# Kernel optimization log

Hardware: AMD Instinct MI355X
Metric: run time of the kernel (lower is better)

## Reference

```python
import jax, jax.numpy as jnp
import numpy as np

N_NODES = 100000


def gcn_conv(x, edge_index, W, b):
    """PyG GCNConv: symmetric normalization with added self-loops.
    x: [N, Fin], edge_index: [2, E], W: [Fin, Fout], b: [Fout]
    """
    n = x.shape[0]
    h = x @ W  # [N, Fout] dense transform first (standard GCNConv order)
    loops = jnp.arange(n, dtype=edge_index.dtype)
    src = jnp.concatenate([edge_index[0], loops])  # self-loops appended
    dst = jnp.concatenate([edge_index[1], loops])
    deg = jax.ops.segment_sum(jnp.ones_like(dst, dtype=h.dtype), dst, num_segments=n)
    dinv = jax.lax.rsqrt(deg)  # deg >= 1 thanks to self-loops
    norm = dinv[src] * dinv[dst]  # [E+N]
    msgs = h[src] * norm[:, None]  # gather + scale
    out = jax.ops.segment_sum(msgs, dst, num_segments=n)  # scatter-add
    return out + b


def setup_inputs() -> dict:
    key = jax.random.key(0)
    k = jax.random.split(key, 9)
    in_c, hid, out_c = 128, 128, 64
    n_edges = 1600000
    x = jax.random.normal(k[0], (N_NODES, in_c), dtype=jnp.float32)
    edge_index = jax.random.randint(k[1], (2, n_edges), 0, N_NODES, dtype=jnp.int64)
    def lin(kw, kb, fan_in, fan_out):
        bound = 1.0 / np.sqrt(fan_in)
        W = jax.random.uniform(kw, (fan_in, fan_out), jnp.float32, -bound, bound)
        b = jax.random.uniform(kb, (fan_out,), jnp.float32, -bound, bound)
        return W, b
    W1, b1 = lin(k[2], k[3], in_c, hid)
    W2, b2 = lin(k[4], k[5], hid, hid)
    Wf, bf = lin(k[6], k[7], hid, out_c)
    return {"x": x, "edge_index": edge_index, "W1": W1, "b1": b1,
            "W2": W2, "b2": b2, "Wf": Wf, "bf": bf}


def reference(x, edge_index, W1, b1, W2, b2, Wf, bf):
    h = jax.nn.relu(gcn_conv(x, edge_index, W1, b1))
    h = jax.nn.relu(gcn_conv(h, edge_index, W2, b2))
    return h @ Wf + bf
```

## Files before the change

kernel.cpp:

```cpp
#include <hip/hip_runtime.h>
#include <stdint.h>

typedef short short8 __attribute__((ext_vector_type(8)));
typedef float floatx4 __attribute__((ext_vector_type(4)));

#define BK 256

static __device__ __forceinline__ float bflo(unsigned int u) {
    union { unsigned int i; float f; } v; v.i = u << 16; return v.f;
}
static __device__ __forceinline__ float bfhi(unsigned int u) {
    union { unsigned int i; float f; } v; v.i = u & 0xffff0000u; return v.f;
}
static __device__ __forceinline__ unsigned short f2bf(float f) {
    union { float f; unsigned int i; } v; v.f = f;
    unsigned int u = v.i;
    unsigned int r = u + 0x7fffu + ((u >> 16) & 1u);
    return (unsigned short)(r >> 16);
}


__global__ void k_zero_cnt(int* bucket_cnt, int K) {
    int i = blockIdx.x * 256 + threadIdx.x;
    if (i < K) bucket_cnt[i] = 0;
}

__global__ __launch_bounds__(256) void k_hist(const int* __restrict__ dst, int* bucket_cnt,
                                              int E, int N, int K) {
    __shared__ int h[512];
    int t = threadIdx.x;
    for (int i = t; i < K; i += 256) h[i] = 0;
    __syncthreads();
    int per = (E + gridDim.x - 1) / gridDim.x;
    int lo = blockIdx.x * per, hi = min(lo + per, E);
    for (int e = lo + t; e < hi; e += 256) {
        unsigned int d = (unsigned int)dst[e];
        if (d < (unsigned int)N) atomicAdd(&h[d >> 8], 1);
    }
    __syncthreads();
    for (int i = t; i < K; i += 256) if (h[i]) atomicAdd(&bucket_cnt[i], h[i]);
}

__global__ void k_scanK(const int* __restrict__ bucket_cnt, int* bucket_off, int* bucket_cur,
                        int* row_start, int K, int N) {
    __shared__ int s[512];
    int t = threadIdx.x;
    int v = (t < K) ? bucket_cnt[t] : 0;
    s[t] = v; __syncthreads();
    for (int off = 1; off < 512; off <<= 1) {
        int x = (t >= off) ? s[t - off] : 0;
        __syncthreads();
        s[t] += x;
        __syncthreads();
    }
    if (t < K) { bucket_off[t] = s[t] - v; bucket_cur[t] = s[t] - v; }
    if (t == K - 1) { bucket_off[K] = s[t]; row_start[N] = s[t]; }
}

__global__ __launch_bounds__(256) void k_binscatter(const int* __restrict__ src,
                                                    const int* __restrict__ dst,
                                                    int* bucket_cur, uint2* __restrict__ tmp,
                                                    int E, int N, int K) {
    __shared__ int h[512];
    __shared__ int base[512];
    int t = threadIdx.x;
    for (int i = t; i < K; i += 256) h[i] = 0;
    __syncthreads();
    int per = (E + gridDim.x - 1) / gridDim.x;
    int lo = blockIdx.x * per, hi = min(lo + per, E);
    for (int e = lo + t; e < hi; e += 256) {
        unsigned int d = (unsigned int)dst[e], sv = (unsigned int)src[e];
        if (d < (unsigned int)N && sv < (unsigned int)N) atomicAdd(&h[d >> 8], 1);
    }
    __syncthreads();
    for (int i = t; i < K; i += 256) {
        int c = h[i];
        base[i] = c ? atomicAdd(&bucket_cur[i], c) : 0;
        h[i] = 0;
    }
    __syncthreads();
    for (int e = lo + t; e < hi; e += 256) {
        unsigned int d = (unsigned int)dst[e], sv = (unsigned int)src[e];
        if (d < (unsigned int)N && sv < (unsigned int)N) {
            int k = d >> 8;
            int p = base[k] + atomicAdd(&h[k], 1);
            tmp[p] = make_uint2(sv, d);
        }
    }
}

__global__ __launch_bounds__(256) void k_fine(const uint2* __restrict__ tmp,
                                              const int* __restrict__ bucket_off,
                                              int* __restrict__ row_start, float* __restrict__ dinv,
                                              int* __restrict__ csr, int N) {
    __shared__ int deg[BK];
    __shared__ int scn[BK];
    __shared__ int cur[BK];
    int b = blockIdx.x;
    int t = threadIdx.x;
    int lo = bucket_off[b], hi = bucket_off[b + 1];
    deg[t] = 0;
    __syncthreads();
    for (int e = lo + t; e < hi; e += 256) {
        int d = tmp[e].y & (BK - 1);
        atomicAdd(&deg[d], 1);
    }
    __syncthreads();
    int v = deg[t];
    scn[t] = v; __syncthreads();
    for (int off = 1; off < 256; off <<= 1) {
        int x = (t >= off) ? scn[t - off] : 0;
        __syncthreads();
        scn[t] += x;
        __syncthreads();
    }
    int rs = lo + scn[t] - v;
    cur[t] = rs;
    int node = b * BK + t;
    if (node < N) { row_start[node] = rs; dinv[node] = rsqrtf((float)(v + 1)); }
    __syncthreads();
    for (int e = lo + t; e < hi; e += 256) {
        uint2 ed = tmp[e];
        int d = ed.y & (BK - 1);
        int p = atomicAdd(&cur[d], 1);
        csr[p] = (int)ed.x;
    }
}


__global__ void k_wconv(const float* __restrict__ W, unsigned short* __restrict__ Wt,
                        int K, int Nc) {
    int i = blockIdx.x * 256 + threadIdx.x;
    if (i < K * Nc) {
        int k = i / Nc, n = i % Nc;
        Wt[n * K + k] = f2bf(W[i]);
    }
}


template <int NOUT, bool SCALE, bool BIAS, bool XF32, bool OUTF32>
__global__ __launch_bounds__(256, 2) void k_gemm(
    const void* __restrict__ Xv, const unsigned short* __restrict__ Wbf,
    const float* __restrict__ bias, const float* __restrict__ dinv,
    void* __restrict__ outv, int M, int MB) {
    __shared__ __align__(16) unsigned short Wl[NOUT * 136];
    int t = threadIdx.x;
    for (int c = t; c < NOUT * 16; c += 256) {
        short8 v = *(const short8*)(Wbf + (size_t)c * 8);
        *(short8*)(&Wl[(c >> 4) * 136 + (c & 15) * 8]) = v;
    }
    __syncthreads();

    int wave = t >> 6, lane = t & 63;
    int quad = lane >> 4, l16 = lane & 15;
    constexpr int NT = NOUT / 16;

    for (int mb = blockIdx.x; mb < MB; mb += gridDim.x) {
        int m0 = mb * 64 + wave * 16;
        int mr = m0 + l16;
        int mrc = mr < M ? mr : M - 1;

        floatx4 acc[NT];
#pragma unroll
        for (int i = 0; i < NT; i++) acc[i] = (floatx4){0.f, 0.f, 0.f, 0.f};

#pragma unroll
        for (int kc = 0; kc < 4; kc++) {
            short8 a;
            if (XF32) {
                const float* X = (const float*)Xv;
                const float* p = X + (size_t)mrc * 128 + kc * 32 + quad * 8;
                float4 xa = *(const float4*)p;
                float4 xb = *(const float4*)(p + 4);
                a[0] = (short)f2bf(xa.x); a[1] = (short)f2bf(xa.y);
                a[2] = (short)f2bf(xa.z); a[3] = (short)f2bf(xa.w);
                a[4] = (short)f2bf(xb.x); a[5] = (short)f2bf(xb.y);
                a[6] = (short)f2bf(xb.z); a[7] = (short)f2bf(xb.w);
            } else {
                const unsigned short* X = (const unsigned short*)Xv;
                a = *(const short8*)(X + (size_t)mrc * 128 + kc * 32 + quad * 8);
            }
#pragma unroll
            for (int nt = 0; nt < NT; nt++) {
                short8 b = *(const short8*)(&Wl[(nt * 16 + l16) * 136 + kc * 32 + quad * 8]);
                acc[nt] = __builtin_amdgcn_mfma_f32_16x16x32_bf16(a, b, acc[nt], 0, 0, 0);
            }
        }

#pragma unroll
        for (int i = 0; i < 4; i++) {
            int r = m0 + quad * 4 + i;
            if (r >= M) continue;
            float sc = SCALE ? dinv[r] : 1.0f;
#pragma unroll
            for (int nt = 0; nt < NT; nt++) {
                int n = nt * 16 + l16;
                float v = acc[nt][i] * sc;
                if (BIAS) v += bias[n];
                if (OUTF32) {
                    ((float*)outv)[(size_t)r * NOUT + n] = v;
                } else {
                    ((unsigned short*)outv)[(size_t)r * NOUT + n] = f2bf(v);
                }
            }
        }
    }
}


__global__ __launch_bounds__(256, 8) void k_aggregate(
    const unsigned short* __restrict__ Hs, const int* __restrict__ csr,
    const int* __restrict__ row_start,
    const float* __restrict__ dinv, const float* __restrict__ bias,
    unsigned short* __restrict__ out, int N, int E) {
    int wave = threadIdx.x >> 6, lane = threadIdx.x & 63;
    int node = blockIdx.x * 4 + wave;
    if (node >= N) return;
    int ch = lane * 2;
    int Nm1 = N - 1;

    unsigned int u = *(const unsigned int*)(Hs + (size_t)node * 128 + ch);
    float a0 = bflo(u), a1 = bfhi(u);

    int e = row_start[node];
    int end = row_start[node + 1];
    if (e < 0) e = 0;
    if (end > E) end = E;

    for (; e + 8 <= end; e += 8) {
        int idx[8];
#pragma unroll
        for (int j = 0; j < 8; j++) idx[j] = __builtin_nontemporal_load(csr + e + j);
        unsigned int uu[8];
#pragma unroll
        for (int j = 0; j < 8; j++) {
            int s = min(max(idx[j], 0), Nm1);
            uu[j] = *(const unsigned int*)(Hs + (size_t)s * 128 + ch);
        }
#pragma unroll
        for (int j = 0; j < 8; j++) { a0 += bflo(uu[j]); a1 += bfhi(uu[j]); }
    }
    if (e + 4 <= end) {
        int idx[4];
#pragma unroll
        for (int j = 0; j < 4; j++) idx[j] = __builtin_nontemporal_load(csr + e + j);
        unsigned int uu[4];
#pragma unroll
        for (int j = 0; j < 4; j++) {
            int s = min(max(idx[j], 0), Nm1);
            uu[j] = *(const unsigned int*)(Hs + (size_t)s * 128 + ch);
        }
#pragma unroll
        for (int j = 0; j < 4; j++) { a0 += bflo(uu[j]); a1 += bfhi(uu[j]); }
        e += 4;
    }
    for (; e < end; e++) {
        int s = min(max(__builtin_nontemporal_load(csr + e), 0), Nm1);
        unsigned int u0 = *(const unsigned int*)(Hs + (size_t)s * 128 + ch);
        a0 += bflo(u0);
        a1 += bfhi(u0);
    }

    float di = dinv[node];
    float r0 = fmaxf(fmaf(di, a0, bias[ch]), 0.f);
    float r1 = fmaxf(fmaf(di, a1, bias[ch + 1]), 0.f);
    unsigned int pk = (unsigned int)f2bf(r0) | ((unsigned int)f2bf(r1) << 16);
    __builtin_nontemporal_store(pk, (unsigned int*)(out + (size_t)node * 128 + ch));
}


extern "C" void kernel_launch(void* const* d_in, const int* in_sizes, int n_in,
                              void* d_out, int out_size, void* d_ws, size_t ws_size,
                              hipStream_t stream) {
    const float* x  = (const float*)d_in[0];
    const int* ei   = (const int*)d_in[1];
    const float* W1 = (const float*)d_in[2];
    const float* b1 = (const float*)d_in[3];
    const float* W2 = (const float*)d_in[4];
    const float* b2 = (const float*)d_in[5];
    const float* Wf = (const float*)d_in[6];
    const float* bf = (const float*)d_in[7];

    int N = in_sizes[0] / 128;
    int E = in_sizes[1] / 2;
    const int* src = ei;
    const int* dst = ei + E;
    int K = (N + BK - 1) / BK;

    size_t need = 0;
    auto pad = [](size_t b) { return (b + 255) & ~(size_t)255; };
    size_t o_bcnt = need; need += pad(512 * 4);
    size_t o_boff = need; need += pad(513 * 4);
    size_t o_bcur = need; need += pad(512 * 4);
    size_t o_rs   = need; need += pad(((size_t)N + 1) * 4);
    size_t o_dinv = need; need += pad((size_t)N * 4);
    size_t o_wbf  = need; need += pad((16384 + 16384 + 8192) * 2);
    size_t o_csr  = need; need += pad((size_t)E * 4);
    size_t o_hs   = need; need += pad((size_t)N * 128 * 2);
    size_t o_a    = need; need += pad((size_t)N * 128 * 2);
    if (ws_size < need) return;
    if ((size_t)E * 8 > (size_t)N * 128 * 2) return;

    char* ws = (char*)d_ws;
    int* bucket_cnt = (int*)(ws + o_bcnt);
    int* bucket_off = (int*)(ws + o_boff);
    int* bucket_cur = (int*)(ws + o_bcur);
    int* row_start  = (int*)(ws + o_rs);
    float* dinv     = (float*)(ws + o_dinv);
    unsigned short* wb1 = (unsigned short*)(ws + o_wbf);
    unsigned short* wb2 = wb1 + 16384;
    unsigned short* wbf = wb2 + 16384;
    int* csr        = (int*)(ws + o_csr);
    unsigned short* Hs = (unsigned short*)(ws + o_hs);
    unsigned short* A  = (unsigned short*)(ws + o_a);
    uint2* tmp      = (uint2*)A;

    k_wconv<<<64, 256, 0, stream>>>(W1, wb1, 128, 128);
    k_wconv<<<64, 256, 0, stream>>>(W2, wb2, 128, 128);
    k_wconv<<<32, 256, 0, stream>>>(Wf, wbf, 128, 64);

    k_zero_cnt<<<(K + 255) / 256, 256, 0, stream>>>(bucket_cnt, K);
    k_hist<<<256, 256, 0, stream>>>(dst, bucket_cnt, E, N, K);
    k_scanK<<<1, 512, 0, stream>>>(bucket_cnt, bucket_off, bucket_cur, row_start, K, N);
    k_binscatter<<<256, 256, 0, stream>>>(src, dst, bucket_cur, tmp, E, N, K);
    k_fine<<<K, 256, 0, stream>>>(tmp, bucket_off, row_start, dinv, csr, N);

    int MB = (N + 63) / 64;
    int GG = (MB + 1) / 2;

    k_gemm<128, true, false, true, false><<<GG, 256, 0, stream>>>(x, wb1, nullptr, dinv, Hs, N, MB);
    k_aggregate<<<(N + 3) / 4, 256, 0, stream>>>(Hs, csr, row_start, dinv, b1, A, N, E);
    k_gemm<128, true, false, false, false><<<GG, 256, 0, stream>>>(A, wb2, nullptr, dinv, Hs, N, MB);
    k_aggregate<<<(N + 3) / 4, 256, 0, stream>>>(Hs, csr, row_start, dinv, b2, A, N, E);
    k_gemm<64, false, true, false, true><<<GG, 256, 0, stream>>>(A, wbf, bf, nullptr, d_out, N, MB);
}
```

Baseline: 376.1 us.

## Pack edge temp to 32-bit, per-wave histograms, vectorized aggregate, fused weight conversion

The aggregate kernel now has each wave handle four edges at once. Each 16-lane group loads 16-byte chunks of a row, and the partial sums are combined with cross-lane shuffles, replacing one 4-byte load per lane per edge. The binning temp buffer is packed into one 32-bit word per edge (source<<8 | local dst) instead of an 8-byte pair, which halves the traffic in binscatter and fine. Histograms use per-wave shared-memory copies to reduce atomic contention. The three weight-conversion launches are merged into one. The shuffle reduction adds ALU work, and the packed format assumes N < 2^24.

```diff
diff --git a/kernel.cpp b/kernel.cpp
--- a/kernel.cpp
+++ b/kernel.cpp
@@ -27,18 +27,21 @@
 
 __global__ __launch_bounds__(256) void k_hist(const int* __restrict__ dst, int* bucket_cnt,
                                               int E, int N, int K) {
-    __shared__ int h[512];
-    int t = threadIdx.x;
-    for (int i = t; i < K; i += 256) h[i] = 0;
+    __shared__ int h[4][512];
+    int t = threadIdx.x, w = t >> 6;
+    for (int i = t; i < 4 * 512; i += 256) ((int*)h)[i] = 0;
     __syncthreads();
     int per = (E + gridDim.x - 1) / gridDim.x;
     int lo = blockIdx.x * per, hi = min(lo + per, E);
     for (int e = lo + t; e < hi; e += 256) {
         unsigned int d = (unsigned int)dst[e];
-        if (d < (unsigned int)N) atomicAdd(&h[d >> 8], 1);
-    }
-    __syncthreads();
-    for (int i = t; i < K; i += 256) if (h[i]) atomicAdd(&bucket_cnt[i], h[i]);
+        if (d < (unsigned int)N) atomicAdd(&h[w][d >> 8], 1);
+    }
+    __syncthreads();
+    for (int i = t; i < K; i += 256) {
+        int c = h[0][i] + h[1][i] + h[2][i] + h[3][i];
+        if (c) atomicAdd(&bucket_cnt[i], c);
+    }
 }
 
 __global__ void k_scanK(const int* __restrict__ bucket_cnt, int* bucket_off, int* bucket_cur,
@@ -59,54 +62,52 @@
 
 __global__ __launch_bounds__(256) void k_binscatter(const int* __restrict__ src,
                                                     const int* __restrict__ dst,
-                                                    int* bucket_cur, uint2* __restrict__ tmp,
+                                                    int* bucket_cur, unsigned int* __restrict__ tmp,
                                                     int E, int N, int K) {
-    __shared__ int h[512];
-    __shared__ int base[512];
-    int t = threadIdx.x;
-    for (int i = t; i < K; i += 256) h[i] = 0;
+    __shared__ int h[4][512];
+    int t = threadIdx.x, w = t >> 6;
+    for (int i = t; i < 4 * 512; i += 256) ((int*)h)[i] = 0;
     __syncthreads();
     int per = (E + gridDim.x - 1) / gridDim.x;
     int lo = blockIdx.x * per, hi = min(lo + per, E);
     for (int e = lo + t; e < hi; e += 256) {
-        unsigned int d = (unsigned int)dst[e], sv = (unsigned int)src[e];
-        if (d < (unsigned int)N && sv < (unsigned int)N) atomicAdd(&h[d >> 8], 1);
-    }
-    __syncthreads();
-    for (int i = t; i < K; i += 256) {
-        int c = h[i];
-        base[i] = c ? atomicAdd(&bucket_cur[i], c) : 0;
-        h[i] = 0;
+        unsigned int d = (unsigned int)dst[e];
+        if (d < (unsigned int)N) atomicAdd(&h[w][d >> 8], 1);
+    }
+    __syncthreads();
+    for (int k = t; k < K; k += 256) {
+        int c0 = h[0][k], c1 = h[1][k], c2 = h[2][k], c3 = h[3][k];
+        int tot = c0 + c1 + c2 + c3;
+        int base = tot ? atomicAdd(&bucket_cur[k], tot) : 0;
+        h[0][k] = base; h[1][k] = base + c0; h[2][k] = base + c0 + c1;
+        h[3][k] = base + c0 + c1 + c2;
     }
     __syncthreads();
     for (int e = lo + t; e < hi; e += 256) {
-        unsigned int d = (unsigned int)dst[e], sv = (unsigned int)src[e];
-        if (d < (unsigned int)N && sv < (unsigned int)N) {
-            int k = d >> 8;
-            int p = base[k] + atomicAdd(&h[k], 1);
-            tmp[p] = make_uint2(sv, d);
+        unsigned int d = (unsigned int)dst[e];
+        if (d < (unsigned int)N) {
+            unsigned int sv = (unsigned int)src[e];
+            if (sv >= (unsigned int)N) sv = 0;
+            int p = atomicAdd(&h[w][d >> 8], 1);
+            tmp[p] = (sv << 8) | (d & 255u);
         }
     }
 }
 
-__global__ __launch_bounds__(256) void k_fine(const uint2* __restrict__ tmp,
+__global__ __launch_bounds__(256) void k_fine(const unsigned int* __restrict__ tmp,
                                               const int* __restrict__ bucket_off,
                                               int* __restrict__ row_start, float* __restrict__ dinv,
                                               int* __restrict__ csr, int N) {
-    __shared__ int deg[BK];
+    __shared__ int deg4[4][BK];
     __shared__ int scn[BK];
     __shared__ int cur[BK];
-    int b = blockIdx.x;
-    int t = threadIdx.x;
+    int b = blockIdx.x, t = threadIdx.x, w = t >> 6;
     int lo = bucket_off[b], hi = bucket_off[b + 1];
-    deg[t] = 0;
-    __syncthreads();
-    for (int e = lo + t; e < hi; e += 256) {
-        int d = tmp[e].y & (BK - 1);
-        atomicAdd(&deg[d], 1);
-    }
-    __syncthreads();
-    int v = deg[t];
+    for (int i = t; i < 4 * BK; i += 256) ((int*)deg4)[i] = 0;
+    __syncthreads();
+    for (int e = lo + t; e < hi; e += 256) atomicAdd(&deg4[w][tmp[e] & 255u], 1);
+    __syncthreads();
+    int v = deg4[0][t] + deg4[1][t] + deg4[2][t] + deg4[3][t];
     scn[t] = v; __syncthreads();
     for (int off = 1; off < 256; off <<= 1) {
         int x = (t >= off) ? scn[t - off] : 0;
@@ -120,20 +121,26 @@
     if (node < N) { row_start[node] = rs; dinv[node] = rsqrtf((float)(v + 1)); }
     __syncthreads();
     for (int e = lo + t; e < hi; e += 256) {
-        uint2 ed = tmp[e];
-        int d = ed.y & (BK - 1);
-        int p = atomicAdd(&cur[d], 1);
-        csr[p] = (int)ed.x;
-    }
-}
-
-
-__global__ void k_wconv(const float* __restrict__ W, unsigned short* __restrict__ Wt,
-                        int K, int Nc) {
+        unsigned int p = tmp[e];
+        int pos = atomicAdd(&cur[p & 255u], 1);
+        csr[pos] = (int)(p >> 8);
+    }
+}
+
+
+__global__ void k_wconv_all(const float* __restrict__ W1, const float* __restrict__ W2,
+                            const float* __restrict__ Wf, unsigned short* __restrict__ wb1,
+                            unsigned short* __restrict__ wb2, unsigned short* __restrict__ wbf) {
     int i = blockIdx.x * 256 + threadIdx.x;
-    if (i < K * Nc) {
-        int k = i / Nc, n = i % Nc;
-        Wt[n * K + k] = f2bf(W[i]);
+    if (i < 16384) {
+        int k = i >> 7, n = i & 127;
+        wb1[n * 128 + k] = f2bf(W1[i]);
+    } else if (i < 32768) {
+        int j = i - 16384, k = j >> 7, n = j & 127;
+        wb2[n * 128 + k] = f2bf(W2[j]);
+    } else if (i < 40960) {
+        int j = i - 32768, k = j >> 6, n = j & 63;
+        wbf[n * 128 + k] = f2bf(Wf[j]);
     }
 }
 
@@ -214,58 +221,79 @@
     const float* __restrict__ dinv, const float* __restrict__ bias,
     unsigned short* __restrict__ out, int N, int E) {
     int wave = threadIdx.x >> 6, lane = threadIdx.x & 63;
+    int grp = lane >> 4, c16 = lane & 15;
     int node = blockIdx.x * 4 + wave;
     if (node >= N) return;
-    int ch = lane * 2;
     int Nm1 = N - 1;
-
-    unsigned int u = *(const unsigned int*)(Hs + (size_t)node * 128 + ch);
-    float a0 = bflo(u), a1 = bfhi(u);
-
-    int e = row_start[node];
+    int cb = c16 * 8;
+
+    float a0 = 0.f, a1 = 0.f, a2 = 0.f, a3 = 0.f, a4 = 0.f, a5 = 0.f, a6 = 0.f, a7 = 0.f;
+
+    int start = row_start[node];
     int end = row_start[node + 1];
-    if (e < 0) e = 0;
+    if (start < 0) start = 0;
     if (end > E) end = E;
-
-    for (; e + 8 <= end; e += 8) {
-        int idx[8];
-#pragma unroll
-        for (int j = 0; j < 8; j++) idx[j] = __builtin_nontemporal_load(csr + e + j);
-        unsigned int uu[8];
-#pragma unroll
-        for (int j = 0; j < 8; j++) {
-            int s = min(max(idx[j], 0), Nm1);
-            uu[j] = *(const unsigned int*)(Hs + (size_t)s * 128 + ch);
-        }
-#pragma unroll
-        for (int j = 0; j < 8; j++) { a0 += bflo(uu[j]); a1 += bfhi(uu[j]); }
-    }
-    if (e + 4 <= end) {
-        int idx[4];
-#pragma unroll
-        for (int j = 0; j < 4; j++) idx[j] = __builtin_nontemporal_load(csr + e + j);
-        unsigned int uu[4];
-#pragma unroll
-        for (int j = 0; j < 4; j++) {
-            int s = min(max(idx[j], 0), Nm1);
-            uu[j] = *(const unsigned int*)(Hs + (size_t)s * 128 + ch);
-        }
-#pragma unroll
-        for (int j = 0; j < 4; j++) { a0 += bflo(uu[j]); a1 += bfhi(uu[j]); }
-        e += 4;
-    }
-    for (; e < end; e++) {
-        int s = min(max(__builtin_nontemporal_load(csr + e), 0), Nm1);
-        unsigned int u0 = *(const unsigned int*)(Hs + (size_t)s * 128 + ch);
-        a0 += bflo(u0);
-        a1 += bfhi(u0);
-    }
+    int cnt = end - start;
+    int full4 = cnt >> 2;
+
+    int it = 0;
+    for (; it + 2 <= full4; it += 2) {
+        int eA = start + it * 4 + grp;
+        int eB = eA + 4;
+        int iA = min(max(csr[eA], 0), Nm1);
+        int iB = min(max(csr[eB], 0), Nm1);
+        uint4 uA = *(const uint4*)(Hs + (size_t)iA * 128 + cb);
+        uint4 uB = *(const uint4*)(Hs + (size_t)iB * 128 + cb);
+        a0 += bflo(uA.x); a1 += bfhi(uA.x); a2 += bflo(uA.y); a3 += bfhi(uA.y);
+        a4 += bflo(uA.z); a5 += bfhi(uA.z); a6 += bflo(uA.w); a7 += bfhi(uA.w);
+        a0 += bflo(uB.x); a1 += bfhi(uB.x); a2 += bflo(uB.y); a3 += bfhi(uB.y);
+        a4 += bflo(uB.z); a5 += bfhi(uB.z); a6 += bflo(uB.w); a7 += bfhi(uB.w);
+    }
+    for (; it < full4; it++) {
+        int eA = start + it * 4 + grp;
+        int iA = min(max(csr[eA], 0), Nm1);
+        uint4 uA = *(const uint4*)(Hs + (size_t)iA * 128 + cb);
+        a0 += bflo(uA.x); a1 += bfhi(uA.x); a2 += bflo(uA.y); a3 += bfhi(uA.y);
+        a4 += bflo(uA.z); a5 += bfhi(uA.z); a6 += bflo(uA.w); a7 += bfhi(uA.w);
+    }
+    int eT = start + full4 * 4 + grp;
+    if (eT < end) {
+        int iT = min(max(csr[eT], 0), Nm1);
+        uint4 uT = *(const uint4*)(Hs + (size_t)iT * 128 + cb);
+        a0 += bflo(uT.x); a1 += bfhi(uT.x); a2 += bflo(uT.y); a3 += bfhi(uT.y);
+        a4 += bflo(uT.z); a5 += bfhi(uT.z); a6 += bflo(uT.w); a7 += bfhi(uT.w);
+    }
+
+    a0 += __shfl_xor(a0, 16); a1 += __shfl_xor(a1, 16); a2 += __shfl_xor(a2, 16);
+    a3 += __shfl_xor(a3, 16); a4 += __shfl_xor(a4, 16); a5 += __shfl_xor(a5, 16);
+    a6 += __shfl_xor(a6, 16); a7 += __shfl_xor(a7, 16);
+    a0 += __shfl_xor(a0, 32); a1 += __shfl_xor(a1, 32); a2 += __shfl_xor(a2, 32);
+    a3 += __shfl_xor(a3, 32); a4 += __shfl_xor(a4, 32); a5 += __shfl_xor(a5, 32);
+    a6 += __shfl_xor(a6, 32); a7 += __shfl_xor(a7, 32);
+
+    uint4 us = *(const uint4*)(Hs + (size_t)node * 128 + cb);
+    a0 += bflo(us.x); a1 += bfhi(us.x); a2 += bflo(us.y); a3 += bfhi(us.y);
+    a4 += bflo(us.z); a5 += bfhi(us.z); a6 += bflo(us.w); a7 += bfhi(us.w);
 
     float di = dinv[node];
-    float r0 = fmaxf(fmaf(di, a0, bias[ch]), 0.f);
-    float r1 = fmaxf(fmaf(di, a1, bias[ch + 1]), 0.f);
-    unsigned int pk = (unsigned int)f2bf(r0) | ((unsigned int)f2bf(r1) << 16);
-    __builtin_nontemporal_store(pk, (unsigned int*)(out + (size_t)node * 128 + ch));
+    float4 b0 = *(const float4*)(bias + cb);
+    float4 b1 = *(const float4*)(bias + cb + 4);
+    float r0 = fmaxf(fmaf(di, a0, b0.x), 0.f);
+    float r1 = fmaxf(fmaf(di, a1, b0.y), 0.f);
+    float r2 = fmaxf(fmaf(di, a2, b0.z), 0.f);
+    float r3 = fmaxf(fmaf(di, a3, b0.w), 0.f);
+    float r4 = fmaxf(fmaf(di, a4, b1.x), 0.f);
+    float r5 = fmaxf(fmaf(di, a5, b1.y), 0.f);
+    float r6 = fmaxf(fmaf(di, a6, b1.z), 0.f);
+    float r7 = fmaxf(fmaf(di, a7, b1.w), 0.f);
+    if (grp == 0) {
+        uint4 o;
+        o.x = (unsigned int)f2bf(r0) | ((unsigned int)f2bf(r1) << 16);
+        o.y = (unsigned int)f2bf(r2) | ((unsigned int)f2bf(r3) << 16);
+        o.z = (unsigned int)f2bf(r4) | ((unsigned int)f2bf(r5) << 16);
+        o.w = (unsigned int)f2bf(r6) | ((unsigned int)f2bf(r7) << 16);
+        *(uint4*)(out + (size_t)node * 128 + cb) = o;
+    }
 }
 
 
@@ -286,6 +314,7 @@
     const int* src = ei;
     const int* dst = ei + E;
     int K = (N + BK - 1) / BK;
+    if (N >= (1 << 24) || K > 512) return;
 
     size_t need = 0;
     auto pad = [](size_t b) { return (b + 255) & ~(size_t)255; };
@@ -299,7 +328,7 @@
     size_t o_hs   = need; need += pad((size_t)N * 128 * 2);
     size_t o_a    = need; need += pad((size_t)N * 128 * 2);
     if (ws_size < need) return;
-    if ((size_t)E * 8 > (size_t)N * 128 * 2) return;
+    if ((size_t)E * 4 > (size_t)N * 128 * 2) return;
 
     char* ws = (char*)d_ws;
     int* bucket_cnt = (int*)(ws + o_bcnt);
@@ -313,13 +342,11 @@
     int* csr        = (int*)(ws + o_csr);
     unsigned short* Hs = (unsigned short*)(ws + o_hs);
     unsigned short* A  = (unsigned short*)(ws + o_a);
-    uint2* tmp      = (uint2*)A;
-
-    k_wconv<<<64, 256, 0, stream>>>(W1, wb1, 128, 128);
-    k_wconv<<<64, 256, 0, stream>>>(W2, wb2, 128, 128);
-    k_wconv<<<32, 256, 0, stream>>>(Wf, wbf, 128, 64);
-
-    k_zero_cnt<<<(K + 255) / 256, 256, 0, stream>>>(bucket_cnt, K);
+    unsigned int* tmp  = (unsigned int*)A;
+
+    k_wconv_all<<<160, 256, 0, stream>>>(W1, W2, Wf, wb1, wb2, wbf);
+
+    k_zero_cnt<<<2, 256, 0, stream>>>(bucket_cnt, 512);
     k_hist<<<256, 256, 0, stream>>>(dst, bucket_cnt, E, N, K);
     k_scanK<<<1, 512, 0, stream>>>(bucket_cnt, bucket_off, bucket_cur, row_start, K, N);
     k_binscatter<<<256, 256, 0, stream>>>(src, dst, bucket_cur, tmp, E, N, K);
```

Measured after the change: 340.8 us. 9.4% less time.
